# Kernel tuning notes

Measured on AMD Instinct MI355X. Metric: run time of the kernel, lower is better.

## Reference

```python
import jax, jax.numpy as jnp
import numpy as np
from jax import lax

N_NODES = 50000
DEG = 32          # fixed degree -> regular graph, matches CSR assumption in gpu2 path
C_IN = 512


def setup_inputs() -> dict:
    key = jax.random.key(0)
    k_x, k_col, k_ea, k_wr, k_wo = jax.random.split(key, 5)
    x = jax.random.normal(k_x, (N_NODES, C_IN), dtype=jnp.float32)
    # edge_index sorted by source with exactly DEG neighbors per node (CSR layout the
    # original code assumes via degree()/cumsum slicing)
    row = jnp.repeat(jnp.arange(N_NODES, dtype=jnp.int32), DEG)
    col = jax.random.randint(k_col, (N_NODES * DEG,), 0, N_NODES, dtype=jnp.int32)
    edge_index = jnp.stack([row, col])                      # [2, E]
    edge_attr = jax.random.normal(k_ea, (N_NODES * DEG,), dtype=jnp.float32)
    batch = jnp.zeros((N_NODES,), dtype=jnp.int32)
    # GraphConv(in_channels, 1): out = agg(x_j) @ w_rel + x @ w_root + b
    w_rel = jax.random.normal(k_wr, (C_IN, 1), dtype=jnp.float32) * 0.02
    w_root = jax.random.normal(k_wo, (C_IN, 1), dtype=jnp.float32) * 0.02
    b = jnp.zeros((1,), dtype=jnp.float32)
    return {"x": x, "edge_index": edge_index, "edge_attr": edge_attr,
            "batch": batch, "w_rel": w_rel, "w_root": w_root, "b": b}


def _greedy_star_clusters(score, nbr):
    """Sequential greedy star contraction (faithful to __merge_stars_with_attr_gpu2__).
    score: [N] node scores, nbr: [N, K] neighbor table (CSR blocks of edge_index[1]).
    Returns cluster ids [N] (int32), center mask [N] (bool), n_clusters (int32)."""
    N = score.shape[0]
    order = jnp.argsort(-score)  # descending, as torch.argsort(descending=True)

    def step(state, v):
        remain, cluster, cnt, center = state
        active = remain[v]
        ds = nbr[v]  # [K] destinations of the star rooted at v
        # cluster[node_idx] = i ; cluster[dests] = i (unconditional overwrite when active)
        cluster = cluster.at[v].set(jnp.where(active, cnt, cluster[v]))
        cluster = cluster.at[ds].set(jnp.where(active, cnt, cluster[ds]))
        remain = remain.at[ds].set(jnp.where(active, False, remain[ds]))
        remain = remain.at[v].set(False)  # v was either already removed or is now a center
        center = center.at[v].set(center[v] | active)
        cnt = cnt + active.astype(jnp.int32)
        return (remain, cluster, cnt, center), None

    init = (jnp.ones((N,), bool), jnp.zeros((N,), jnp.int32),
            jnp.int32(0), jnp.zeros((N,), bool))
    (_, cluster, cnt, center), _ = lax.scan(step, init, order)
    return cluster, center, cnt


def reference(x, edge_index, edge_attr, batch, w_rel, w_root, b):
    N, _ = x.shape
    src, dst = edge_index[0], edge_index[1]
    # GraphConv score (add-aggregation of source features into targets)
    agg = jax.ops.segment_sum(x[src], dst, num_segments=N)      # [N, C]
    score = jnp.tanh(agg @ w_rel + x @ w_root + b).reshape(-1)  # [N]

    nbr = dst.reshape(N, DEG)  # regular CSR: row i holds neighbors of node i
    cluster, center, n_clusters = _greedy_star_clusters(score, nbr)

    # scatter_add of node features into clusters; rows >= n_clusters are zero padding
    new_x = jax.ops.segment_sum(x, cluster, num_segments=N)     # [N, C] (padded)
    new_edge_index = cluster[edge_index]                         # coarsened edges (uncoalesced)
    new_batch = jnp.zeros((N,), batch.dtype).at[cluster].set(batch)
    return (new_x, new_edge_index, edge_attr, new_batch, cluster, center, n_clusters)
```

## Files before the change

### kernel.cpp

```cpp
#include <hip/hip_runtime.h>

#define NN   50000
#define NE   1600000
#define CIN  512
#define CCAP 16384
#define IN_STR 96
#define E_STR  72
#define OVF   (1 << 30)
#define MAX_PASS 100000

#define ST_UNK 0
#define ST_CEN 1
#define ST_REM 2

#define RPW 8

#define SC_GROUPS 8
#define SC_PER (NN / SC_GROUPS)
#define SC_BLK_PER_G 128

__device__ __forceinline__ bool earlier_f(double zu, int u, double zv, int v) {
    return (zu > zv) || (zu == zv && u < v);
}

__device__ __forceinline__ int ld_state(const int* p) {
    return __hip_atomic_load(p, __ATOMIC_RELAXED, __HIP_MEMORY_SCOPE_AGENT);
}
__device__ __forceinline__ void st_state(int* p, int v) {
    __hip_atomic_store(p, v, __ATOMIC_RELAXED, __HIP_MEMORY_SCOPE_AGENT);
}

__global__ __launch_bounds__(256) void k_rowdots(const float* __restrict__ x,
                                                 const float* __restrict__ wrel,
                                                 const float* __restrict__ wroot,
                                                 const float* __restrict__ bptr,
                                                 double* __restrict__ p,
                                                 double* __restrict__ z) {
    int wave = (blockIdx.x * blockDim.x + threadIdx.x) >> 6;
    int lane = threadIdx.x & 63;
    if (wave >= NN) return;
    const float4* xr = (const float4*)(x + (size_t)wave * CIN);
    const float4* wr = (const float4*)wrel;
    const float4* wo = (const float4*)wroot;
    double pd = 0.0, qd = 0.0;
    int i0 = lane * 2;
#pragma unroll
    for (int k = 0; k < 2; ++k) {
        float4 xv = xr[i0 + k];
        float4 wv = wr[i0 + k];
        float4 ov = wo[i0 + k];
        pd += (double)xv.x * wv.x + (double)xv.y * wv.y + (double)xv.z * wv.z + (double)xv.w * wv.w;
        qd += (double)xv.x * ov.x + (double)xv.y * ov.y + (double)xv.z * ov.z + (double)xv.w * ov.w;
    }
    for (int off = 32; off > 0; off >>= 1) {
        pd += __shfl_down(pd, off);
        qd += __shfl_down(qd, off);
    }
    if (lane == 0) {
        p[wave] = pd;
        z[wave] = qd + (double)bptr[0];
    }
}

__global__ __launch_bounds__(256) void k_scatter(const int* __restrict__ src, const int* __restrict__ dst,
                                                 int* __restrict__ cnt, int* __restrict__ inSrc) {
    int g = blockIdx.x & (SC_GROUPS - 1);
    int sub = blockIdx.x >> 3;
    int lo = g * SC_PER, hi = lo + SC_PER;
    for (int e = sub * 256 + threadIdx.x; e < NE; e += SC_BLK_PER_G * 256) {
        int t = dst[e];
        if (t >= lo && t < hi) {
            int pos = atomicAdd(&cnt[t], 1);
            if (pos < IN_STR) inSrc[(size_t)t * IN_STR + pos] = src[e];
        }
    }
}

__global__ __launch_bounds__(256) void k_zacc(double* __restrict__ z, const double* __restrict__ p,
                                              const int* __restrict__ cnt, const int* __restrict__ inSrc) {
    int v = blockIdx.x * blockDim.x + threadIdx.x;
    if (v >= NN) return;
    int deg = min(cnt[v], IN_STR);
    size_t b = (size_t)v * IN_STR;
    double acc = z[v];
    for (int i = 0; i < deg; ++i) acc += p[inSrc[b + i]];
    z[v] = acc;
}

__global__ __launch_bounds__(256) void k_prep(const double* __restrict__ z, const int* __restrict__ cnt,
                                              const int* __restrict__ inSrc,
                                              int* __restrict__ eNbr, int* __restrict__ eCnt) {
    int v = blockIdx.x * blockDim.x + threadIdx.x;
    if (v >= NN) return;
    double zv = z[v];
    int deg = min(cnt[v], IN_STR);
    size_t b = (size_t)v * IN_STR;
    size_t eb = (size_t)v * E_STR;
    int c = 0;
    bool ovf = false;
    for (int i = 0; i < deg; ++i) {
        int u = inSrc[b + i];
        if (earlier_f(z[u], u, zv, v)) {
            if (c < E_STR) eNbr[eb + c] = u;
            else ovf = true;
            ++c;
        }
    }
    eCnt[v] = ovf ? OVF : c;
}

__global__ __launch_bounds__(256) void k_fix_spin(const double* __restrict__ z,
                                                  const int* __restrict__ cnt, const int* __restrict__ inSrc,
                                                  int* __restrict__ eNbr, int* __restrict__ eCnt,
                                                  int* __restrict__ state) {
    int v = blockIdx.x * blockDim.x + threadIdx.x;
    bool active = (v < NN);
    bool ovf = false;
    int c = 0;
    size_t eb = 0;
    unsigned long long m0 = 0ull, m1 = 0ull;
    int deg = 0;
    size_t b = 0;

    if (active) {
        c = eCnt[v];
        eb = (size_t)v * E_STR;
        if (c >= OVF) {
            ovf = true;
            double zv = z[v];
            deg = min(cnt[v], IN_STR);
            b = (size_t)v * IN_STR;
            for (int i = 0; i < deg; ++i) {
                int u = inSrc[b + i];
                if (earlier_f(z[u], u, zv, v)) {
                    if (i < 64) m0 |= 1ull << i; else m1 |= 1ull << (i - 64);
                }
            }
        }
    }

    int pass = 0;
    while (active) {
        bool rem = false;
        bool resolved = false;
        if (!ovf) {
            int w = 0;
            for (int j = 0; j < c && !rem; j += 8) {
                int m = c - j; if (m > 8) m = 8;
                int us[8], ss[8];
#pragma unroll
                for (int k = 0; k < 8; ++k) if (k < m) us[k] = eNbr[eb + j + k];
#pragma unroll
                for (int k = 0; k < 8; ++k) if (k < m) ss[k] = ld_state(&state[us[k]]);
#pragma unroll
                for (int k = 0; k < 8; ++k) {
                    if (k < m) {
                        if (ss[k] == ST_CEN) rem = true;
                        else if (ss[k] == ST_UNK) eNbr[eb + (w++)] = us[k];
                    }
                }
            }
            if (rem) resolved = true;
            else { c = w; if (c == 0) resolved = true; }
        } else {
            for (int i = 0; i < deg; ++i) {
                bool live = (i < 64) ? ((m0 >> i) & 1ull) : ((m1 >> (i - 64)) & 1ull);
                if (!live) continue;
                int u = inSrc[b + i];
                int st = ld_state(&state[u]);
                if (st == ST_CEN) { rem = true; break; }
                if (st == ST_REM) {
                    if (i < 64) m0 &= ~(1ull << i); else m1 &= ~(1ull << (i - 64));
                }
            }
            if (rem || !(m0 | m1)) resolved = true;
        }
        if (++pass >= MAX_PASS) resolved = true;
        if (resolved) {
            st_state(&state[v], rem ? ST_REM : ST_CEN);
            active = false;
        } else {
            __builtin_amdgcn_s_sleep(2);
        }
    }
}

__global__ __launch_bounds__(256) void k_compact(const int* __restrict__ state, const double* __restrict__ z,
                                                 double* __restrict__ cz, int* __restrict__ cidx,
                                                 int* counters) {
    int v = blockIdx.x * blockDim.x + threadIdx.x;
    if (v >= NN) return;
    if (state[v] == ST_CEN) {
        int slot = atomicAdd(&counters[0], 1);
        if (slot < CCAP) { cz[slot] = z[v]; cidx[slot] = v; }
    }
}

__global__ __launch_bounds__(256) void k_rank(const double* __restrict__ cz, const int* __restrict__ cidx,
                                              const int* __restrict__ counters, int* __restrict__ cidOfNode) {
    __shared__ double tz[2048];
    __shared__ int ti[2048];
    int C = counters[0];
    if (C > CCAP) C = CCAP;
    int blockBase = blockIdx.x * (256 / 64) * RPW;
    if (blockBase >= C) return;
    int lane = threadIdx.x & 63;
    int wv = blockBase / RPW + (threadIdx.x >> 6);
    int g0 = wv * RPW;
    double myz[RPW];
    int myi[RPW];
    int r[RPW];
#pragma unroll
    for (int k = 0; k < RPW; ++k) {
        int g = g0 + k;
        bool m = (g < C);
        myz[k] = m ? cz[g] : 0.0;
        myi[k] = m ? cidx[g] : 0;
        r[k] = 0;
    }
    for (int base = 0; base < C; base += 2048) {
        int tile = min(2048, C - base);
        for (int t = threadIdx.x; t < tile; t += 256) { tz[t] = cz[base + t]; ti[t] = cidx[base + t]; }
        __syncthreads();
        for (int t = lane; t < tile; t += 64) {
            double zt = tz[t];
            int it = ti[t];
#pragma unroll
            for (int k = 0; k < RPW; ++k)
                if (earlier_f(zt, it, myz[k], myi[k])) ++r[k];
        }
        __syncthreads();
    }
#pragma unroll
    for (int k = 0; k < RPW; ++k) {
        int rr = r[k];
        for (int off = 32; off > 0; off >>= 1) rr += __shfl_down(rr, off);
        if (lane == 0) {
            int g = g0 + k;
            if (g < C && myi[k] >= 0 && myi[k] < NN) cidOfNode[myi[k]] = rr;
        }
    }
}

__global__ __launch_bounds__(256) void k_assign(const int* __restrict__ state, const double* __restrict__ z,
                                                const int* __restrict__ cnt, const int* __restrict__ inSrc,
                                                const int* __restrict__ cidOfNode, const int* __restrict__ batch,
                                                float* __restrict__ out_cl,
                                                float* __restrict__ out_ce, float* __restrict__ out_nb,
                                                int* __restrict__ mCount) {
    int u = blockIdx.x * blockDim.x + threadIdx.x;
    if (u >= NN) return;
    bool have = false;
    double bz = 0.0;
    int bi = -1;
    int stu = state[u];
    if (stu == ST_CEN) { have = true; bz = z[u]; bi = u; }
    int deg = min(cnt[u], IN_STR);
    size_t b = (size_t)u * IN_STR;
    for (int i = 0; i < deg; ++i) {
        int w = inSrc[b + i];
        if (state[w] != ST_CEN) continue;
        double zw = z[w];
        if (!have || earlier_f(bz, bi, zw, w)) { have = true; bz = zw; bi = w; }
    }
    int cl = have ? cidOfNode[bi] : 0;
    if (cl < 0) cl = 0;
    if (cl >= CCAP) cl = CCAP - 1;
    out_cl[u] = (float)cl;
    out_ce[u] = (stu == ST_CEN) ? 1.0f : 0.0f;
    out_nb[cl] = (float)batch[u];
    atomicAdd(&mCount[cl], 1);
}

__global__ __launch_bounds__(1024) void k_scan(const int* __restrict__ in, int* __restrict__ out,
                                               int* __restrict__ cur, int n) {
    __shared__ int wsum[16];
    __shared__ int wpre[16];
    int tid = threadIdx.x, lane = tid & 63, wid = tid >> 6;
    int running = 0;
    for (int base = 0; base < n; base += 1024) {
        int i = base + tid;
        int v = (i < n) ? in[i] : 0;
        int incl = v;
        for (int off = 1; off < 64; off <<= 1) {
            int t = __shfl_up(incl, off);
            if (lane >= off) incl += t;
        }
        if (lane == 63) wsum[wid] = incl;
        __syncthreads();
        if (wid == 0 && lane < 16) {
            int s = wsum[lane];
            for (int off = 1; off < 16; off <<= 1) {
                int t = __shfl_up(s, off);
                if (lane >= off) s += t;
            }
            wpre[lane] = s - wsum[lane];
        }
        __syncthreads();
        int excl = running + wpre[wid] + incl - v;
        if (i < n) { out[i] = excl; if (cur) cur[i] = excl; }
        int tot = wpre[15] + wsum[15];
        running += tot;
        __syncthreads();
    }
    if (tid == 0) out[n] = running;
}

__global__ __launch_bounds__(256) void k_members(const float* __restrict__ out_cl, int* __restrict__ mCursor,
                                                 int* __restrict__ members) {
    int u = blockIdx.x * blockDim.x + threadIdx.x;
    if (u < NN) {
        int cl = (int)out_cl[u];
        if (cl < 0) cl = 0;
        if (cl >= CCAP) cl = CCAP - 1;
        int pos = atomicAdd(&mCursor[cl], 1);
        if (pos >= 0 && pos < NN) members[pos] = u;
    }
}

__global__ __launch_bounds__(256) void k_newx(const float* __restrict__ x, const int* __restrict__ mStart,
                                              const int* __restrict__ members, const int* __restrict__ counters,
                                              float* __restrict__ out_x) {
    int b = blockIdx.x;
    int t = threadIdx.x;
    int C = counters[0];
    if (C > CCAP) C = CCAP;
    double a0 = 0.0, a1 = 0.0;
    if (b < C) {
        int s = mStart[b], e = mStart[b + 1];
        for (int m = s; m < e; ++m) {
            const float* row = x + (size_t)members[m] * CIN;
            a0 += (double)row[t];
            a1 += (double)row[t + 256];
        }
    }
    out_x[(size_t)b * CIN + t] = (float)a0;
    out_x[(size_t)b * CIN + t + 256] = (float)a1;
}

__global__ __launch_bounds__(256) void k_edges(const int* __restrict__ src, const int* __restrict__ dst,
                                               const float* __restrict__ attr, const float* __restrict__ out_cl,
                                               float* __restrict__ out_ei, float* __restrict__ out_at) {
    int e = blockIdx.x * blockDim.x + threadIdx.x;
    if (e >= NE) return;
    int s = src[e], d = dst[e];
    float cs = (s >= 0 && s < NN) ? out_cl[s] : 0.0f;
    float cd = (d >= 0 && d < NN) ? out_cl[d] : 0.0f;
    out_ei[e] = cs;
    out_ei[NE + e] = cd;
    out_at[e] = attr[e];
}

__global__ void k_final(const int* counters, float* out_nc) {
    if (threadIdx.x == 0 && blockIdx.x == 0) {
        int C = counters[0];
        if (C > CCAP) C = CCAP;
        out_nc[0] = (float)C;
    }
}

extern "C" void kernel_launch(void* const* d_in, const int* in_sizes, int n_in,
                              void* d_out, int out_size, void* d_ws, size_t ws_size,
                              hipStream_t stream) {
    const float* x = (const float*)d_in[0];
    const int* ei = (const int*)d_in[1];
    const float* ea = (const float*)d_in[2];
    const int* batch = (const int*)d_in[3];
    const float* wrel = (const float*)d_in[4];
    const float* wroot = (const float*)d_in[5];
    const float* bptr = (const float*)d_in[6];
    float* out = (float*)d_out;
    (void)d_ws; (void)ws_size; (void)in_sizes; (void)n_in; (void)out_size;

    const int* src = ei;
    const int* dst = ei + NE;

    float* out_x = out;
    float* out_ei = out + (size_t)NN * CIN;
    float* out_at = out_ei + 2 * (size_t)NE;
    float* out_nb = out_at + (size_t)NE;
    float* out_cl = out_nb + NN;
    float* out_ce = out_cl + NN;
    float* out_nc = out_ce + NN;

    char* r1 = (char*)out_x;
    size_t off1 = 0;
    auto alloc1 = [&](size_t bytes) -> void* {
        void* ptr = (void*)(r1 + off1);
        off1 = (off1 + bytes + 255) & ~(size_t)255;
        return ptr;
    };
    double* p_ = (double*)alloc1(NN * 8);
    double* z_ = (double*)alloc1(NN * 8);
    double* cz = (double*)alloc1(CCAP * 8);
    int* cnt = (int*)alloc1(NN * 4);
    int* state = (int*)alloc1(NN * 4);
    int* cidOfNode = (int*)alloc1(NN * 4);
    int* cidx = (int*)alloc1(CCAP * 4);
    int* eCnt = (int*)alloc1(NN * 4);
    int* inSrc = (int*)alloc1((size_t)NN * IN_STR * 4);
    int* eNbr = (int*)alloc1((size_t)NN * E_STR * 4);

    char* r2 = (char*)out_at;
    size_t off2 = 0;
    auto alloc2 = [&](size_t bytes) -> void* {
        void* ptr = (void*)(r2 + off2);
        off2 = (off2 + bytes + 255) & ~(size_t)255;
        return ptr;
    };
    int* members = (int*)alloc2(NN * 4);
    int* mCount = (int*)alloc2(CCAP * 4);
    int* mStart = (int*)alloc2((CCAP + 1) * 4);
    int* mCursor = (int*)alloc2(CCAP * 4);
    int* counters = (int*)alloc2(64);

    hipMemsetAsync(cnt, 0, NN * 4, stream);
    hipMemsetAsync(state, 0, NN * 4, stream);
    hipMemsetAsync(mCount, 0, CCAP * 4, stream);
    hipMemsetAsync(counters, 0, 64, stream);
    hipMemsetAsync(out_nb, 0, NN * 4, stream);

    const int TB = 256;
    const int GN = (NN + TB - 1) / TB;
    const int GE = (NE + TB - 1) / TB;

    k_rowdots<<<(NN * 64 + TB - 1) / TB, TB, 0, stream>>>(x, wrel, wroot, bptr, p_, z_);
    k_scatter<<<SC_GROUPS * SC_BLK_PER_G, TB, 0, stream>>>(src, dst, cnt, inSrc);
    k_zacc<<<GN, TB, 0, stream>>>(z_, p_, cnt, inSrc);
    k_prep<<<GN, TB, 0, stream>>>(z_, cnt, inSrc, eNbr, eCnt);

    {
        void* coopArgs[] = { (void*)&z_, (void*)&cnt, (void*)&inSrc,
                             (void*)&eNbr, (void*)&eCnt, (void*)&state };
        hipLaunchCooperativeKernel((const void*)k_fix_spin, dim3(GN), dim3(TB),
                                   coopArgs, 0, stream);
    }

    k_compact<<<GN, TB, 0, stream>>>(state, z_, cz, cidx, counters);
    k_rank<<<CCAP / (RPW * 4), TB, 0, stream>>>(cz, cidx, counters, cidOfNode);
    k_assign<<<GN, TB, 0, stream>>>(state, z_, cnt, inSrc, cidOfNode, batch,
                                    out_cl, out_ce, out_nb, mCount);
    k_scan<<<1, 1024, 0, stream>>>(mCount, mStart, mCursor, CCAP);
    k_members<<<GN, TB, 0, stream>>>(out_cl, mCursor, members);
    k_newx<<<NN, TB, 0, stream>>>(x, mStart, members, counters, out_x);
    k_final<<<1, 64, 0, stream>>>(counters, out_nc);
    k_edges<<<GE, TB, 0, stream>>>(src, dst, ea, out_cl, out_ei, out_at);
}
```

Measured before the change: 629.7 us.

## Partition edges by destination group before scatter; fuse compaction and count into neighbors

The old scatter had every block group scan all edges and keep only those whose destination fell in its range, so the edge list was read eight times. A new partition kernel bins each edge tile into 8 destination groups in shared memory and appends them to per-group staging buffers. A second pass then does the atomic inSrc fill while reading each edge only once. Center compaction now happens inside the cooperative spin kernel, and the cluster-count write moves into k_rank, which removes two small launches. The cost is an extra staging buffer and kernel, plus a fixed per-group capacity that could overflow on skewed inputs.

```diff
diff --git a/kernel.cpp b/kernel.cpp
--- a/kernel.cpp
+++ b/kernel.cpp
@@ -18,6 +18,9 @@
 #define SC_GROUPS 8
 #define SC_PER (NN / SC_GROUPS)
 #define SC_BLK_PER_G 128
+#define SC_TILE 2048
+#define SC_ABLK ((NE + SC_TILE - 1) / SC_TILE)
+#define SC_CAP 400000
 
 __device__ __forceinline__ bool earlier_f(double zu, int u, double zv, int v) {
     return (zu > zv) || (zu == zv && u < v);
@@ -62,17 +65,58 @@
     }
 }
 
-__global__ __launch_bounds__(256) void k_scatter(const int* __restrict__ src, const int* __restrict__ dst,
-                                                 int* __restrict__ cnt, int* __restrict__ inSrc) {
+__global__ __launch_bounds__(256) void k_part(const int* __restrict__ src, const int* __restrict__ dst,
+                                              int2* __restrict__ stage, int* __restrict__ gCnt) {
+    __shared__ int2 bins[SC_GROUPS][512];
+    __shared__ int lcnt[SC_GROUPS];
+    __shared__ int gbase[SC_GROUPS];
+    int tid = threadIdx.x;
+    if (tid < SC_GROUPS) lcnt[tid] = 0;
+    __syncthreads();
+    int e0 = blockIdx.x * SC_TILE;
+#pragma unroll
+    for (int k = 0; k < SC_TILE / 256; ++k) {
+        int e = e0 + k * 256 + tid;
+        if (e < NE) {
+            int d = dst[e];
+            if (d >= 0 && d < NN) {
+                int g = d / SC_PER;
+                int pos = atomicAdd(&lcnt[g], 1);
+                if (pos < 512) bins[g][pos] = make_int2(d, src[e]);
+                else {
+                    int gp = atomicAdd(&gCnt[g], 1);
+                    if (gp < SC_CAP) stage[(size_t)g * SC_CAP + gp] = make_int2(d, src[e]);
+                }
+            }
+        }
+    }
+    __syncthreads();
+    if (tid < SC_GROUPS) {
+        int c = min(lcnt[tid], 512);
+        gbase[tid] = atomicAdd(&gCnt[tid], c);
+        lcnt[tid] = c;
+    }
+    __syncthreads();
+    for (int g = 0; g < SC_GROUPS; ++g) {
+        int c = lcnt[g], b = gbase[g];
+        for (int i = tid; i < c; i += 256) {
+            int idx = b + i;
+            if (idx < SC_CAP) stage[(size_t)g * SC_CAP + idx] = bins[g][i];
+        }
+    }
+}
+
+__global__ __launch_bounds__(256) void k_scatter2(const int2* __restrict__ stage, const int* __restrict__ gCnt,
+                                                  int* __restrict__ cnt, int* __restrict__ inSrc) {
     int g = blockIdx.x & (SC_GROUPS - 1);
     int sub = blockIdx.x >> 3;
-    int lo = g * SC_PER, hi = lo + SC_PER;
-    for (int e = sub * 256 + threadIdx.x; e < NE; e += SC_BLK_PER_G * 256) {
-        int t = dst[e];
-        if (t >= lo && t < hi) {
-            int pos = atomicAdd(&cnt[t], 1);
-            if (pos < IN_STR) inSrc[(size_t)t * IN_STR + pos] = src[e];
-        }
+    int n = gCnt[g];
+    if (n > SC_CAP) n = SC_CAP;
+    const int2* s = stage + (size_t)g * SC_CAP;
+    for (int i = sub * 256 + threadIdx.x; i < n; i += SC_BLK_PER_G * 256) {
+        int2 ds = s[i];
+        int pos = atomicAdd(&cnt[ds.x], 1);
+        if (pos < IN_STR) inSrc[(size_t)ds.x * IN_STR + pos] = ds.y;
     }
 }
 
@@ -112,7 +156,9 @@
 __global__ __launch_bounds__(256) void k_fix_spin(const double* __restrict__ z,
                                                   const int* __restrict__ cnt, const int* __restrict__ inSrc,
                                                   int* __restrict__ eNbr, int* __restrict__ eCnt,
-                                                  int* __restrict__ state) {
+                                                  int* __restrict__ state,
+                                                  double* __restrict__ cz, int* __restrict__ cidx,
+                                                  int* __restrict__ counters) {
     int v = blockIdx.x * blockDim.x + threadIdx.x;
     bool active = (v < NN);
     bool ovf = false;
@@ -178,6 +224,10 @@
         if (++pass >= MAX_PASS) resolved = true;
         if (resolved) {
             st_state(&state[v], rem ? ST_REM : ST_CEN);
+            if (!rem) {
+                int slot = atomicAdd(&counters[0], 1);
+                if (slot < CCAP) { cz[slot] = z[v]; cidx[slot] = v; }
+            }
             active = false;
         } else {
             __builtin_amdgcn_s_sleep(2);
@@ -185,23 +235,14 @@
     }
 }
 
-__global__ __launch_bounds__(256) void k_compact(const int* __restrict__ state, const double* __restrict__ z,
-                                                 double* __restrict__ cz, int* __restrict__ cidx,
-                                                 int* counters) {
-    int v = blockIdx.x * blockDim.x + threadIdx.x;
-    if (v >= NN) return;
-    if (state[v] == ST_CEN) {
-        int slot = atomicAdd(&counters[0], 1);
-        if (slot < CCAP) { cz[slot] = z[v]; cidx[slot] = v; }
-    }
-}
-
 __global__ __launch_bounds__(256) void k_rank(const double* __restrict__ cz, const int* __restrict__ cidx,
-                                              const int* __restrict__ counters, int* __restrict__ cidOfNode) {
+                                              const int* __restrict__ counters, int* __restrict__ cidOfNode,
+                                              float* __restrict__ out_nc) {
     __shared__ double tz[2048];
     __shared__ int ti[2048];
     int C = counters[0];
     if (C > CCAP) C = CCAP;
+    if (blockIdx.x == 0 && threadIdx.x == 0) out_nc[0] = (float)C;
     int blockBase = blockIdx.x * (256 / 64) * RPW;
     if (blockBase >= C) return;
     int lane = threadIdx.x & 63;
@@ -351,14 +392,6 @@
     out_at[e] = attr[e];
 }
 
-__global__ void k_final(const int* counters, float* out_nc) {
-    if (threadIdx.x == 0 && blockIdx.x == 0) {
-        int C = counters[0];
-        if (C > CCAP) C = CCAP;
-        out_nc[0] = (float)C;
-    }
-}
-
 extern "C" void kernel_launch(void* const* d_in, const int* in_sizes, int n_in,
                               void* d_out, int out_size, void* d_ws, size_t ws_size,
                               hipStream_t stream) {
@@ -400,6 +433,7 @@
     int* eCnt = (int*)alloc1(NN * 4);
     int* inSrc = (int*)alloc1((size_t)NN * IN_STR * 4);
     int* eNbr = (int*)alloc1((size_t)NN * E_STR * 4);
+    int2* stage = (int2*)alloc1((size_t)SC_GROUPS * SC_CAP * 8);
 
     char* r2 = (char*)out_at;
     size_t off2 = 0;
@@ -423,26 +457,27 @@
     const int TB = 256;
     const int GN = (NN + TB - 1) / TB;
     const int GE = (NE + TB - 1) / TB;
+    int* gCnt = counters + 8;
 
     k_rowdots<<<(NN * 64 + TB - 1) / TB, TB, 0, stream>>>(x, wrel, wroot, bptr, p_, z_);
-    k_scatter<<<SC_GROUPS * SC_BLK_PER_G, TB, 0, stream>>>(src, dst, cnt, inSrc);
+    k_part<<<SC_ABLK, TB, 0, stream>>>(src, dst, stage, gCnt);
+    k_scatter2<<<SC_GROUPS * SC_BLK_PER_G, TB, 0, stream>>>(stage, gCnt, cnt, inSrc);
     k_zacc<<<GN, TB, 0, stream>>>(z_, p_, cnt, inSrc);
     k_prep<<<GN, TB, 0, stream>>>(z_, cnt, inSrc, eNbr, eCnt);
 
     {
         void* coopArgs[] = { (void*)&z_, (void*)&cnt, (void*)&inSrc,
-                             (void*)&eNbr, (void*)&eCnt, (void*)&state };
+                             (void*)&eNbr, (void*)&eCnt, (void*)&state,
+                             (void*)&cz, (void*)&cidx, (void*)&counters };
         hipLaunchCooperativeKernel((const void*)k_fix_spin, dim3(GN), dim3(TB),
                                    coopArgs, 0, stream);
     }
 
-    k_compact<<<GN, TB, 0, stream>>>(state, z_, cz, cidx, counters);
-    k_rank<<<CCAP / (RPW * 4), TB, 0, stream>>>(cz, cidx, counters, cidOfNode);
+    k_rank<<<CCAP / (RPW * 4), TB, 0, stream>>>(cz, cidx, counters, cidOfNode, out_nc);
     k_assign<<<GN, TB, 0, stream>>>(state, z_, cnt, inSrc, cidOfNode, batch,
                                     out_cl, out_ce, out_nb, mCount);
     k_scan<<<1, 1024, 0, stream>>>(mCount, mStart, mCursor, CCAP);
     k_members<<<GN, TB, 0, stream>>>(out_cl, mCursor, members);
     k_newx<<<NN, TB, 0, stream>>>(x, mStart, members, counters, out_x);
-    k_final<<<1, 64, 0, stream>>>(counters, out_nc);
     k_edges<<<GE, TB, 0, stream>>>(src, dst, ea, out_cl, out_ei, out_at);
 }
```

Measured after the change: 630.2 us. No clear change (+0.1%).
